# Performance work log

Measured on AMD Instinct MI355X. Metric: run time of the kernel, lower is better.

The kernel has to match this reference:

```python
import jax, jax.numpy as jnp
import numpy as np

B, T, DEMO = 64, 4096, 8
N_MOD, N_POS = 37, 10
D_IN = N_POS + 1 + N_MOD  # 48
PHI_W, LATENT = 128, 128
PSI_W, PSI_L = 128, 128
DOT, HEADS = 64, 4
RHO_W, OUT = 128, 1
MAX_TIME = 1000.0


def _dense_init(key, fan_in, fan_out):
    lim = float(np.sqrt(6.0 / fan_in))  # he_uniform-ish
    return jax.random.uniform(key, (fan_in, fan_out), jnp.float32, -lim, lim)


def setup_inputs() -> dict:
    key = jax.random.key(0)
    ks = jax.random.split(key, 32)
    inp = {}
    inp['demo'] = jax.random.normal(ks[0], (B, DEMO), jnp.float32)
    inp['times'] = jax.random.uniform(ks[1], (B, T, 1), jnp.float32, 0.0, 100.0)
    inp['values'] = jax.random.normal(ks[2], (B, T, 1), jnp.float32)
    inp['measurements'] = jax.random.randint(ks[3], (B, T), 0, N_MOD, jnp.int32)
    # all sequences full length -> N = B*(T+1) static
    inp['segment_ids'] = jnp.repeat(jnp.arange(B, dtype=jnp.int32), T + 1)
    inp['timescales'] = jnp.asarray(MAX_TIME ** np.linspace(0.0, 1.0, N_POS // 2), jnp.float32)
    inp['demo_W1'] = _dense_init(ks[4], DEMO, PHI_W); inp['demo_b1'] = jnp.zeros((PHI_W,), jnp.float32)
    inp['demo_W2'] = _dense_init(ks[5], PHI_W, D_IN); inp['demo_b2'] = jnp.zeros((D_IN,), jnp.float32)
    dims = [D_IN, PHI_W, PHI_W, PHI_W, LATENT]
    for i in range(4):
        inp['phi_W%d' % i] = _dense_init(ks[6 + i], dims[i], dims[i + 1])
        inp['phi_b%d' % i] = jnp.zeros((dims[i + 1],), jnp.float32)
    pdims = [D_IN, PSI_W, PSI_W, PSI_L]
    for i in range(3):
        inp['psi_W%d' % i] = _dense_init(ks[10 + i], pdims[i], pdims[i + 1])
        inp['psi_b%d' % i] = jnp.zeros((pdims[i + 1],), jnp.float32)
    inp['W_k'] = _dense_init(ks[13], PSI_L + D_IN, DOT * HEADS)
    # original inits W_q to zeros (degenerate uniform attention); small random keeps test non-trivial
    inp['W_q'] = jax.random.normal(ks[14], (HEADS, DOT), jnp.float32) * 0.05
    rdims = [LATENT * HEADS, RHO_W, RHO_W, RHO_W, OUT]
    for i in range(4):
        inp['rho_W%d' % i] = _dense_init(ks[15 + i], rdims[i], rdims[i + 1])
        inp['rho_b%d' % i] = jnp.zeros((rdims[i + 1],), jnp.float32)
    return inp


def _forward(demo, times, values, timescales,
             demo_W1, demo_b1, demo_W2, demo_b2,
             phi_W0, phi_b0, phi_W1, phi_b1, phi_W2, phi_b2, phi_W3, phi_b3,
             psi_W0, psi_b0, psi_W1, psi_b1, psi_W2, psi_b2,
             W_k, W_q,
             rho_W0, rho_b0, rho_W1, rho_b1, rho_W2, rho_b2, rho_W3, rho_b3,
             measurements, segment_ids):
    relu = jax.nn.relu
    nseg = demo.shape[0]
    # positional encoding: times [B,T,1] / timescales [5] -> sin|cos -> [B,T,10]
    scaled = times / timescales[None, None, :]
    tt = jnp.concatenate([jnp.sin(scaled), jnp.cos(scaled)], axis=-1)
    meas = jax.nn.one_hot(measurements, N_MOD, dtype=times.dtype)  # [B,T,37]
    combined = jnp.concatenate([tt, values, meas], axis=-1)        # [B,T,48]
    demo_enc = relu(demo @ demo_W1 + demo_b1) @ demo_W2 + demo_b2  # [B,48]
    x = jnp.concatenate([demo_enc[:, None, :], combined], axis=1)  # [B,T+1,48]
    collected = x.reshape(-1, x.shape[-1])                         # [N,48]
    # phi MLP -> encoded [N,LATENT]
    h = collected
    for W, b in ((phi_W0, phi_b0), (phi_W1, phi_b1), (phi_W2, phi_b2), (phi_W3, phi_b3)):
        h = relu(h @ W + b)
    encoded = h
    # psi MLP -> [N,PSI_L], then per-segment mean, scattered back
    p = collected
    for W, b in ((psi_W0, psi_b0), (psi_W1, psi_b1), (psi_W2, psi_b2)):
        p = relu(p @ W + b)
    seg_sum = jax.ops.segment_sum(p, segment_ids, num_segments=nseg)
    counts = jax.ops.segment_sum(jnp.ones((p.shape[0],), p.dtype), segment_ids, num_segments=nseg)
    agg = seg_sum / counts[:, None]
    comb2 = jnp.concatenate([collected, agg[segment_ids]], axis=-1)  # [N, 48+128]
    keys = (comb2 @ W_k).reshape(-1, HEADS, DOT)                     # [N,H,D]
    preattn = jnp.einsum('nhd,hd->nh', keys, W_q) / jnp.sqrt(jnp.float32(DOT))
    # segment softmax per head
    m = jax.ops.segment_max(preattn, segment_ids, num_segments=nseg)
    e = jnp.exp(preattn - m[segment_ids])
    s = jax.ops.segment_sum(e, segment_ids, num_segments=nseg)
    attn = e / s[segment_ids]                                        # [N,H]
    # head-major weighted concat: [N, H*LATENT]
    weighted = (attn[:, :, None] * encoded[:, None, :]).reshape(-1, HEADS * LATENT)
    agg_out = jax.ops.segment_sum(weighted, segment_ids, num_segments=nseg)  # [B,512]
    r = agg_out
    for W, b in ((rho_W0, rho_b0), (rho_W1, rho_b1), (rho_W2, rho_b2)):
        r = relu(r @ W + b)
    return jax.nn.sigmoid(r @ rho_W3 + rho_b3)  # [B,1]


def reference(demo, times, values, timescales,
              demo_W1, demo_b1, demo_W2, demo_b2,
              phi_W0, phi_b0, phi_W1, phi_b1, phi_W2, phi_b2, phi_W3, phi_b3,
              psi_W0, psi_b0, psi_W1, psi_b1, psi_W2, psi_b2,
              W_k, W_q,
              rho_W0, rho_b0, rho_W1, rho_b1, rho_W2, rho_b2, rho_W3, rho_b3,
              measurements, segment_ids):
    return _forward(demo, times, values, timescales,
                    demo_W1, demo_b1, demo_W2, demo_b2,
                    phi_W0, phi_b0, phi_W1, phi_b1, phi_W2, phi_b2, phi_W3, phi_b3,
                    psi_W0, psi_b0, psi_W1, psi_b1, psi_W2, psi_b2,
                    W_k, W_q,
                    rho_W0, rho_b0, rho_W1, rho_b1, rho_W2, rho_b2, rho_W3, rho_b3,
                    measurements, segment_ids)
```

## Files before the change

kernel.cpp:

```cpp
#include <hip/hip_runtime.h>
#include <hip/hip_bf16.h>
#include <math.h>


#define BSEG 64
#define TLEN 4096
#define NPART 9
#define PART_STRIDE 520

#define OFF_DEMO 0
#define OFF_WQ   3072
#define OFF_WT   3264
#define OFF_PARTIALS 31936

typedef __attribute__((ext_vector_type(8))) short short8;
typedef __attribute__((ext_vector_type(4))) float f32x4;

static __device__ __forceinline__ float bfbits2f(unsigned v) { return __uint_as_float(v << 16); }
static __device__ __forceinline__ unsigned short f2bf_rne(float x) {
  unsigned u = __float_as_uint(x);
  unsigned r = (u + 0x7FFFu + ((u >> 16) & 1u)) >> 16;
  return (unsigned short)r;
}
static __device__ __forceinline__ unsigned pk2(float a, float b) {
  float2 f2 = make_float2(a, b);
  __hip_bfloat162 h = __float22bfloat162_rn(f2);
  unsigned u;
  __builtin_memcpy(&u, &h, 4);
  return u;
}

__global__ __launch_bounds__(256) void k_prep(
    const float* __restrict__ demo, const float* __restrict__ dW1, const float* __restrict__ db1,
    const float* __restrict__ dW2, const float* __restrict__ db2,
    const float* __restrict__ Wk, const float* __restrict__ Wq,
    const float* __restrict__ W0, const float* __restrict__ W1,
    const float* __restrict__ W2, const float* __restrict__ W3,
    float* __restrict__ ws) {
  __shared__ float drow[8];
  __shared__ float hdrow[128];
  int bid = blockIdx.x, tid = threadIdx.x;
  if (bid < 224) {
    unsigned short* wt = (unsigned short*)(ws + OFF_WT);
    int i = bid * 256 + tid;
    float v;
    if (i < 8192) {
      int n = i >> 6, k = i & 63;
      v = (k < 48) ? W0[k * 128 + n] : 0.f;
    } else {
      int j = i - 8192;
      int l = j >> 14, r = j & 16383;
      int n = r >> 7, k = r & 127;
      const float* W = (l == 0) ? W1 : (l == 1) ? W2 : W3;
      v = W[k * 128 + n];
    }
    wt[i] = f2bf_rne(v);
    return;
  }
  if (bid == 224) {
    if (tid < 192) {
      int i = tid >> 2, h = tid & 3;
      float a = 0.f;
      for (int d = 0; d < 64; ++d) a = fmaf(Wk[i * 256 + h * 64 + d], Wq[h * 64 + d], a);
      ws[OFF_WQ + tid] = a * 0.125f;
    }
    return;
  }
  int r = bid - 225;
  if (tid < 8) drow[tid] = demo[r * 8 + tid];
  __syncthreads();
  if (tid < 128) {
    float a = db1[tid];
#pragma unroll
    for (int i = 0; i < 8; ++i) a = fmaf(drow[i], dW1[i * 128 + tid], a);
    hdrow[tid] = fmaxf(a, 0.f);
  }
  __syncthreads();
  if (tid < 48) {
    float a = db2[tid];
    for (int k = 0; k < 128; ++k) a = fmaf(hdrow[k], dW2[k * 48 + tid], a);
    ws[OFF_DEMO + r * 48 + tid] = a;
  }
}

static __device__ __forceinline__ void mfma_layer(
    const unsigned short* hin, unsigned short* hout,
    const short8 (&Bf)[2][4], const float (&bias)[2],
    int l16, int quad, int n0) {
#pragma unroll
  for (int mt = 0; mt < 4; ++mt) {
    short8 A[4];
#pragma unroll
    for (int s = 0; s < 4; ++s)
      A[s] = *(const short8*)(hin + (mt * 16 + l16) * 136 + s * 32 + quad * 8);
#pragma unroll
    for (int t = 0; t < 2; ++t) {
      f32x4 acc = {bias[t], bias[t], bias[t], bias[t]};
#pragma unroll
      for (int s = 0; s < 4; ++s)
        acc = __builtin_amdgcn_mfma_f32_16x16x32_bf16(A[s], Bf[t][s], acc, 0, 0, 0);
      int col = n0 + t * 16 + l16;
      int base = (mt * 16 + quad * 4) * 136 + col;
      unsigned u01 = pk2(fmaxf(acc[0], 0.f), fmaxf(acc[1], 0.f));
      unsigned u23 = pk2(fmaxf(acc[2], 0.f), fmaxf(acc[3], 0.f));
      hout[base]           = (unsigned short)u01;
      hout[base + 136]     = (unsigned short)(u01 >> 16);
      hout[base + 2 * 136] = (unsigned short)u23;
      hout[base + 3 * 136] = (unsigned short)(u23 >> 16);
    }
  }
}
static __device__ __forceinline__ void mfma_layer0(
    const unsigned short* cin, unsigned short* hout,
    const short8 (&B0)[2][2], const float (&bias0)[2],
    int l16, int quad, int n0) {
#pragma unroll
  for (int mt = 0; mt < 4; ++mt) {
    short8 A0[2];
#pragma unroll
    for (int s = 0; s < 2; ++s)
      A0[s] = *(const short8*)(cin + (mt * 16 + l16) * 72 + s * 32 + quad * 8);
#pragma unroll
    for (int t = 0; t < 2; ++t) {
      f32x4 acc = {bias0[t], bias0[t], bias0[t], bias0[t]};
      acc = __builtin_amdgcn_mfma_f32_16x16x32_bf16(A0[0], B0[t][0], acc, 0, 0, 0);
      acc = __builtin_amdgcn_mfma_f32_16x16x32_bf16(A0[1], B0[t][1], acc, 0, 0, 0);
      int col = n0 + t * 16 + l16;
      int base = (mt * 16 + quad * 4) * 136 + col;
      unsigned u01 = pk2(fmaxf(acc[0], 0.f), fmaxf(acc[1], 0.f));
      unsigned u23 = pk2(fmaxf(acc[2], 0.f), fmaxf(acc[3], 0.f));
      hout[base]           = (unsigned short)u01;
      hout[base + 136]     = (unsigned short)(u01 >> 16);
      hout[base + 2 * 136] = (unsigned short)u23;
      hout[base + 3 * 136] = (unsigned short)(u23 >> 16);
    }
  }
}

__global__ __launch_bounds__(256, 2) void k_main(
    const float* __restrict__ times, const float* __restrict__ values,
    const int* __restrict__ meas, const float* __restrict__ tsc,
    const float* __restrict__ ws,
    const float* __restrict__ b0g, const float* __restrict__ b1g,
    const float* __restrict__ b2g, const float* __restrict__ b3g,
    float* __restrict__ part) {
  __shared__ __align__(16) unsigned short hA[64 * 136];
  __shared__ __align__(16) unsigned short hB[64 * 136];
  __shared__ __align__(16) float elds[256];
  __shared__ float wql[192];
  int tid = threadIdx.x;
  const int lane = tid & 63, wv = tid >> 6, quad = lane >> 4, l16 = lane & 15;
  const int n0 = wv * 32;

  const unsigned short* wt = (const unsigned short*)(ws + OFF_WT);
  short8 B0[2][2], B1[2][4], B2[2][4], B3[2][4];
  float bias0[2], bias1[2], bias2[2], bias3[2];
#pragma unroll
  for (int t = 0; t < 2; ++t) {
    int n = n0 + t * 16 + l16;
    bias0[t] = b0g[n]; bias1[t] = b1g[n]; bias2[t] = b2g[n]; bias3[t] = b3g[n];
#pragma unroll
    for (int s = 0; s < 2; ++s)
      B0[t][s] = *(const short8*)(wt + n * 64 + s * 32 + quad * 8);
#pragma unroll
    for (int s = 0; s < 4; ++s) {
      B1[t][s] = *(const short8*)(wt + 8192  + n * 128 + s * 32 + quad * 8);
      B2[t][s] = *(const short8*)(wt + 24576 + n * 128 + s * 32 + quad * 8);
      B3[t][s] = *(const short8*)(wt + 40960 + n * 128 + s * 32 + quad * 8);
    }
  }
  if (tid < 192) wql[tid] = ws[OFF_WQ + tid];
  __syncthreads();

  if (blockIdx.x == 512) {
    {
      int r = tid >> 2, cs = tid & 3;
      unsigned short seg[16];
#pragma unroll
      for (int i = 0; i < 16; ++i) seg[i] = 0;
      if (cs < 3)
#pragma unroll
        for (int i = 0; i < 16; ++i) seg[i] = f2bf_rne(ws[OFF_DEMO + r * 48 + cs * 16 + i]);
      unsigned u[8];
#pragma unroll
      for (int i = 0; i < 8; ++i) u[i] = (unsigned)seg[2 * i] | ((unsigned)seg[2 * i + 1] << 16);
      uint4* dst = (uint4*)(hB + r * 72 + cs * 16);
      dst[0] = make_uint4(u[0], u[1], u[2], u[3]);
      dst[1] = make_uint4(u[4], u[5], u[6], u[7]);
    }
    {
      int r = tid >> 2, h = tid & 3;
      float a = 0.f;
      for (int i = 0; i < 48; ++i) a = fmaf(ws[OFF_DEMO + r * 48 + i], wql[i * 4 + h], a);
      elds[tid] = __expf(a);
    }
    __syncthreads();
    mfma_layer0(hB, hA, B0, bias0, l16, quad, n0); __syncthreads();
    mfma_layer(hA, hB, B1, bias1, l16, quad, n0); __syncthreads();
    mfma_layer(hB, hA, B2, bias2, l16, quad, n0); __syncthreads();
    mfma_layer(hA, hB, B3, bias3, l16, quad, n0); __syncthreads();
    {
      int r = tid >> 2, h = tid & 3;
      part[(r * NPART + 8) * PART_STRIDE + 4 + h] = elds[tid];
    }
    for (int i = tid; i < 64 * 512; i += 256) {
      int r = i >> 9, rem = i & 511;
      int h = rem >> 7, l = rem & 127;
      part[(r * NPART + 8) * PART_STRIDE + 8 + rem] =
          elds[r * 4 + h] * bfbits2f(hB[r * 136 + l]);
    }
    return;
  }

  int b = blockIdx.x >> 3, c = blockIdx.x & 7;
  int t0 = c << 9;
  float invts[5];
#pragma unroll
  for (int i = 0; i < 5; ++i) invts[i] = 1.f / tsc[i];

  float pacc[2][4] = {{0.f, 0.f, 0.f, 0.f}, {0.f, 0.f, 0.f, 0.f}};
  float sacc[4] = {0.f, 0.f, 0.f, 0.f};
  for (int tile = 0; tile < 8; ++tile) {
    int rb = tile << 6;
    {
      int r = tid >> 2, cs = tid & 3;
      int t = t0 + rb + r;
      int mm = meas[b * TLEN + t];
      unsigned short seg[16];
#pragma unroll
      for (int i = 0; i < 16; ++i) seg[i] = 0;
      if (cs == 0) {
        float tv = times[b * TLEN + t];
        float vvv = values[b * TLEN + t];
        float f[11];
#pragma unroll
        for (int i = 0; i < 5; ++i) {
          float s = tv * invts[i];
          f[i] = __sinf(s); f[5 + i] = __cosf(s);
          seg[i] = f2bf_rne(f[i]); seg[5 + i] = f2bf_rne(f[5 + i]);
        }
        f[10] = vvv;
        seg[10] = f2bf_rne(vvv);
#pragma unroll
        for (int h = 0; h < 4; ++h) {
          float a = wql[(11 + mm) * 4 + h];
#pragma unroll
          for (int i = 0; i < 11; ++i) a = fmaf(f[i], wql[i * 4 + h], a);
          elds[r * 4 + h] = __expf(a);
        }
      }
      int kk = 11 + mm;
      if ((kk >> 4) == cs) seg[kk & 15] = 0x3F80;
      unsigned u[8];
#pragma unroll
      for (int i = 0; i < 8; ++i) u[i] = (unsigned)seg[2 * i] | ((unsigned)seg[2 * i + 1] << 16);
      uint4* dst = (uint4*)(hB + r * 72 + cs * 16);
      dst[0] = make_uint4(u[0], u[1], u[2], u[3]);
      dst[1] = make_uint4(u[4], u[5], u[6], u[7]);
    }
    __syncthreads();
    mfma_layer0(hB, hA, B0, bias0, l16, quad, n0); __syncthreads();
    mfma_layer(hA, hB, B1, bias1, l16, quad, n0); __syncthreads();
    mfma_layer(hB, hA, B2, bias2, l16, quad, n0); __syncthreads();
#pragma unroll
    for (int mt = 0; mt < 4; ++mt) {
      short8 A[4];
#pragma unroll
      for (int s = 0; s < 4; ++s)
        A[s] = *(const short8*)(hA + (mt * 16 + l16) * 136 + s * 32 + quad * 8);
      f32x4 acc0 = {bias3[0], bias3[0], bias3[0], bias3[0]};
      f32x4 acc1 = {bias3[1], bias3[1], bias3[1], bias3[1]};
#pragma unroll
      for (int s = 0; s < 4; ++s) {
        acc0 = __builtin_amdgcn_mfma_f32_16x16x32_bf16(A[s], B3[0][s], acc0, 0, 0, 0);
        acc1 = __builtin_amdgcn_mfma_f32_16x16x32_bf16(A[s], B3[1][s], acc1, 0, 0, 0);
      }
#pragma unroll
      for (int j = 0; j < 4; ++j) {
        int lr = mt * 16 + quad * 4 + j;
        float4 e4 = *(const float4*)(elds + lr * 4);
        float v0 = fmaxf(acc0[j], 0.f), v1 = fmaxf(acc1[j], 0.f);
        pacc[0][0] = fmaf(v0, e4.x, pacc[0][0]);
        pacc[0][1] = fmaf(v0, e4.y, pacc[0][1]);
        pacc[0][2] = fmaf(v0, e4.z, pacc[0][2]);
        pacc[0][3] = fmaf(v0, e4.w, pacc[0][3]);
        pacc[1][0] = fmaf(v1, e4.x, pacc[1][0]);
        pacc[1][1] = fmaf(v1, e4.y, pacc[1][1]);
        pacc[1][2] = fmaf(v1, e4.z, pacc[1][2]);
        pacc[1][3] = fmaf(v1, e4.w, pacc[1][3]);
        sacc[0] += e4.x; sacc[1] += e4.y; sacc[2] += e4.z; sacc[3] += e4.w;
      }
    }
    __syncthreads();
  }
#pragma unroll
  for (int t = 0; t < 2; ++t)
#pragma unroll
    for (int h = 0; h < 4; ++h) {
      float v = pacc[t][h];
      v += __shfl_xor(v, 16, 64);
      v += __shfl_xor(v, 32, 64);
      pacc[t][h] = v;
    }
#pragma unroll
  for (int h = 0; h < 4; ++h) {
    float v = sacc[h];
    v += __shfl_xor(v, 16, 64);
    v += __shfl_xor(v, 32, 64);
    sacc[h] = v;
  }
  float* P = part + (b * NPART + c) * PART_STRIDE;
  if (tid < 4) P[4 + tid] = sacc[tid];
  if (quad == 0)
#pragma unroll
    for (int t = 0; t < 2; ++t)
#pragma unroll
      for (int h = 0; h < 4; ++h)
        P[8 + h * 128 + (n0 + t * 16 + l16)] = pacc[t][h];
}

__global__ __launch_bounds__(256) void k_combine(
    const float* __restrict__ part,
    const float* __restrict__ rW0, const float* __restrict__ rb0,
    const float* __restrict__ rW1, const float* __restrict__ rb1,
    const float* __restrict__ rW2, const float* __restrict__ rb2,
    const float* __restrict__ rW3, const float* __restrict__ rb3,
    float* __restrict__ out) {
  __shared__ float Ss[4], agg[512], r1[128], p0[256];
  int tid = threadIdx.x;
  int b = blockIdx.x;
  const float* P = part + b * NPART * PART_STRIDE;
  if (tid < 4) {
    float s = 0.f;
    for (int p = 0; p < NPART; ++p) s += P[p * PART_STRIDE + 4 + tid];
    Ss[tid] = s;
  }
  __syncthreads();
  for (int idx = tid; idx < 512; idx += 256) {
    int h = idx >> 7;
    float a = 0.f;
    for (int p = 0; p < NPART; ++p) a += P[p * PART_STRIDE + 8 + idx];
    agg[idx] = a / Ss[h];
  }
  __syncthreads();
  const int col = tid & 127, half = tid >> 7;
  {
    float a = 0.f;
    for (int k = half * 256; k < half * 256 + 256; ++k) a = fmaf(agg[k], rW0[k * 128 + col], a);
    p0[tid] = a;
  }
  __syncthreads();
  if (tid < 128) r1[tid] = fmaxf(rb0[tid] + p0[tid] + p0[128 + tid], 0.f);
  __syncthreads();
  {
    float a = 0.f;
    for (int k = half * 64; k < half * 64 + 64; ++k) a = fmaf(r1[k], rW1[k * 128 + col], a);
    p0[tid] = a;
  }
  __syncthreads();
  if (tid < 128) r1[tid] = fmaxf(rb1[tid] + p0[tid] + p0[128 + tid], 0.f);
  __syncthreads();
  {
    float a = 0.f;
    for (int k = half * 64; k < half * 64 + 64; ++k) a = fmaf(r1[k], rW2[k * 128 + col], a);
    p0[tid] = a;
  }
  __syncthreads();
  if (tid < 128) p0[tid] = fmaxf(rb2[tid] + p0[tid] + p0[128 + tid], 0.f) * rW3[tid];
  __syncthreads();
  if (tid < 64) {
    float v = p0[tid] + p0[tid + 64];
#pragma unroll
    for (int off = 32; off > 0; off >>= 1) v += __shfl_xor(v, off, 64);
    if (tid == 0) out[b] = 1.f / (1.f + __expf(-(rb3[0] + v)));
  }
}

extern "C" void kernel_launch(void* const* d_in, const int* in_sizes, int n_in,
                              void* d_out, int out_size, void* d_ws, size_t ws_size,
                              hipStream_t stream) {
  const float* demo   = (const float*)d_in[0];
  const float* times  = (const float*)d_in[1];
  const float* values = (const float*)d_in[2];
  const int*   meas   = (const int*)d_in[3];
  const float* tsc = (const float*)d_in[5];
  const float* dW1 = (const float*)d_in[6];
  const float* db1 = (const float*)d_in[7];
  const float* dW2 = (const float*)d_in[8];
  const float* db2 = (const float*)d_in[9];
  const float* pW0 = (const float*)d_in[10];
  const float* pb0 = (const float*)d_in[11];
  const float* pW1 = (const float*)d_in[12];
  const float* pb1 = (const float*)d_in[13];
  const float* pW2 = (const float*)d_in[14];
  const float* pb2 = (const float*)d_in[15];
  const float* pW3 = (const float*)d_in[16];
  const float* pb3 = (const float*)d_in[17];
  const float* Wk  = (const float*)d_in[24];
  const float* Wq  = (const float*)d_in[25];
  const float* rW0 = (const float*)d_in[26];
  const float* rb0 = (const float*)d_in[27];
  const float* rW1 = (const float*)d_in[28];
  const float* rb1 = (const float*)d_in[29];
  const float* rW2 = (const float*)d_in[30];
  const float* rb2 = (const float*)d_in[31];
  const float* rW3 = (const float*)d_in[32];
  const float* rb3 = (const float*)d_in[33];
  float* ws = (float*)d_ws;
  float* partials = ws + OFF_PARTIALS;

  k_prep<<<289, 256, 0, stream>>>(demo, dW1, db1, dW2, db2, Wk, Wq,
                                  pW0, pW1, pW2, pW3, ws);
  k_main<<<513, 256, 0, stream>>>(times, values, meas, tsc, ws,
                                  pb0, pb1, pb2, pb3, partials);
  k_combine<<<64, 256, 0, stream>>>(partials, rW0, rb0, rW1, rb1, rW2, rb2, rW3, rb3,
                                    (float*)d_out);
}
```

Before: 193.5 us.

## Precompute attention weights upfront and double-buffer layer-0 input tile construction

All 512 attention exponentials per block are computed in a prologue using all 256 threads, replacing the per-tile computation done by one thread in four. The per-block denominator sums are now reduced across the whole workgroup. The layer-0 input tile is double-buffered: the next tile is built while the current layer-0 MFMA runs, which also removes one barrier per tile. The cost is about 18 KB of extra LDS per block, which may lower occupancy below the two blocks per CU the launch bounds ask for, plus a prologue that reads the global inputs a second time.

```diff
diff --git a/kernel.cpp b/kernel.cpp
--- a/kernel.cpp
+++ b/kernel.cpp
@@ -146,8 +146,11 @@
     float* __restrict__ part) {
   __shared__ __align__(16) unsigned short hA[64 * 136];
   __shared__ __align__(16) unsigned short hB[64 * 136];
-  __shared__ __align__(16) float elds[256];
+  __shared__ __align__(16) unsigned short c0a[64 * 72];
+  __shared__ __align__(16) unsigned short c0b[64 * 72];
+  __shared__ __align__(16) float preb[512 * 4];
   __shared__ float wql[192];
+  __shared__ float mred[16];
   int tid = threadIdx.x;
   const int lane = tid & 63, wv = tid >> 6, quad = lane >> 4, l16 = lane & 15;
   const int n0 = wv * 32;
@@ -184,7 +187,7 @@
       unsigned u[8];
 #pragma unroll
       for (int i = 0; i < 8; ++i) u[i] = (unsigned)seg[2 * i] | ((unsigned)seg[2 * i + 1] << 16);
-      uint4* dst = (uint4*)(hB + r * 72 + cs * 16);
+      uint4* dst = (uint4*)(c0a + r * 72 + cs * 16);
       dst[0] = make_uint4(u[0], u[1], u[2], u[3]);
       dst[1] = make_uint4(u[4], u[5], u[6], u[7]);
     }
@@ -192,22 +195,22 @@
       int r = tid >> 2, h = tid & 3;
       float a = 0.f;
       for (int i = 0; i < 48; ++i) a = fmaf(ws[OFF_DEMO + r * 48 + i], wql[i * 4 + h], a);
-      elds[tid] = __expf(a);
+      preb[tid] = __expf(a);
     }
     __syncthreads();
-    mfma_layer0(hB, hA, B0, bias0, l16, quad, n0); __syncthreads();
+    mfma_layer0(c0a, hA, B0, bias0, l16, quad, n0); __syncthreads();
     mfma_layer(hA, hB, B1, bias1, l16, quad, n0); __syncthreads();
     mfma_layer(hB, hA, B2, bias2, l16, quad, n0); __syncthreads();
     mfma_layer(hA, hB, B3, bias3, l16, quad, n0); __syncthreads();
     {
       int r = tid >> 2, h = tid & 3;
-      part[(r * NPART + 8) * PART_STRIDE + 4 + h] = elds[tid];
+      part[(r * NPART + 8) * PART_STRIDE + 4 + h] = preb[tid];
     }
     for (int i = tid; i < 64 * 512; i += 256) {
       int r = i >> 9, rem = i & 511;
       int h = rem >> 7, l = rem & 127;
       part[(r * NPART + 8) * PART_STRIDE + 8 + rem] =
-          elds[r * 4 + h] * bfbits2f(hB[r * 136 + l]);
+          preb[r * 4 + h] * bfbits2f(hB[r * 136 + l]);
     }
     return;
   }
@@ -218,48 +221,67 @@
 #pragma unroll
   for (int i = 0; i < 5; ++i) invts[i] = 1.f / tsc[i];
 
+  float s4[4] = {0.f, 0.f, 0.f, 0.f};
+  for (int rr = 0; rr < 2; ++rr) {
+    int r = tid + rr * 256;
+    int t = t0 + r;
+    float tv = times[b * TLEN + t];
+    float vvv = values[b * TLEN + t];
+    int mm = meas[b * TLEN + t];
+    float f[11];
+#pragma unroll
+    for (int i = 0; i < 5; ++i) { float s = tv * invts[i]; f[i] = __sinf(s); f[5 + i] = __cosf(s); }
+    f[10] = vvv;
+#pragma unroll
+    for (int h = 0; h < 4; ++h) {
+      float a = wql[(11 + mm) * 4 + h];
+#pragma unroll
+      for (int i = 0; i < 11; ++i) a = fmaf(f[i], wql[i * 4 + h], a);
+      float e = __expf(a);
+      preb[r * 4 + h] = e;
+      s4[h] += e;
+    }
+  }
+
+#define BUILD_TILE(buf, rbase)                                                  \
+  do {                                                                          \
+    int r_ = tid >> 2, cs_ = tid & 3;                                           \
+    int t_ = t0 + (rbase) + r_;                                                 \
+    int mm_ = meas[b * TLEN + t_];                                              \
+    unsigned short seg_[16];                                                    \
+    _Pragma("unroll") for (int i_ = 0; i_ < 16; ++i_) seg_[i_] = 0;             \
+    if (cs_ == 0) {                                                             \
+      float tv_ = times[b * TLEN + t_];                                         \
+      float vv_ = values[b * TLEN + t_];                                        \
+      _Pragma("unroll") for (int i_ = 0; i_ < 5; ++i_) {                        \
+        float s_ = tv_ * invts[i_];                                             \
+        seg_[i_] = f2bf_rne(__sinf(s_)); seg_[5 + i_] = f2bf_rne(__cosf(s_));   \
+      }                                                                         \
+      seg_[10] = f2bf_rne(vv_);                                                 \
+    }                                                                           \
+    int kk_ = 11 + mm_;                                                         \
+    if ((kk_ >> 4) == cs_) seg_[kk_ & 15] = 0x3F80;                             \
+    unsigned u_[8];                                                             \
+    _Pragma("unroll") for (int i_ = 0; i_ < 8; ++i_)                            \
+      u_[i_] = (unsigned)seg_[2 * i_] | ((unsigned)seg_[2 * i_ + 1] << 16);     \
+    uint4* dst_ = (uint4*)((buf) + r_ * 72 + cs_ * 16);                         \
+    dst_[0] = make_uint4(u_[0], u_[1], u_[2], u_[3]);                           \
+    dst_[1] = make_uint4(u_[4], u_[5], u_[6], u_[7]);                           \
+  } while (0)
+
+  BUILD_TILE(c0a, 0);
+
   float pacc[2][4] = {{0.f, 0.f, 0.f, 0.f}, {0.f, 0.f, 0.f, 0.f}};
-  float sacc[4] = {0.f, 0.f, 0.f, 0.f};
   for (int tile = 0; tile < 8; ++tile) {
     int rb = tile << 6;
-    {
-      int r = tid >> 2, cs = tid & 3;
-      int t = t0 + rb + r;
-      int mm = meas[b * TLEN + t];
-      unsigned short seg[16];
-#pragma unroll
-      for (int i = 0; i < 16; ++i) seg[i] = 0;
-      if (cs == 0) {
-        float tv = times[b * TLEN + t];
-        float vvv = values[b * TLEN + t];
-        float f[11];
-#pragma unroll
-        for (int i = 0; i < 5; ++i) {
-          float s = tv * invts[i];
-          f[i] = __sinf(s); f[5 + i] = __cosf(s);
-          seg[i] = f2bf_rne(f[i]); seg[5 + i] = f2bf_rne(f[5 + i]);
-        }
-        f[10] = vvv;
-        seg[10] = f2bf_rne(vvv);
-#pragma unroll
-        for (int h = 0; h < 4; ++h) {
-          float a = wql[(11 + mm) * 4 + h];
-#pragma unroll
-          for (int i = 0; i < 11; ++i) a = fmaf(f[i], wql[i * 4 + h], a);
-          elds[r * 4 + h] = __expf(a);
-        }
-      }
-      int kk = 11 + mm;
-      if ((kk >> 4) == cs) seg[kk & 15] = 0x3F80;
-      unsigned u[8];
-#pragma unroll
-      for (int i = 0; i < 8; ++i) u[i] = (unsigned)seg[2 * i] | ((unsigned)seg[2 * i + 1] << 16);
-      uint4* dst = (uint4*)(hB + r * 72 + cs * 16);
-      dst[0] = make_uint4(u[0], u[1], u[2], u[3]);
-      dst[1] = make_uint4(u[4], u[5], u[6], u[7]);
-    }
     __syncthreads();
-    mfma_layer0(hB, hA, B0, bias0, l16, quad, n0); __syncthreads();
+    const unsigned short* cin = (tile & 1) ? c0b : c0a;
+    mfma_layer0(cin, hA, B0, bias0, l16, quad, n0);
+    if (tile < 7) {
+      unsigned short* nbuf = (tile & 1) ? c0a : c0b;
+      BUILD_TILE(nbuf, rb + 64);
+    }
+    __syncthreads();
     mfma_layer(hA, hB, B1, bias1, l16, quad, n0); __syncthreads();
     mfma_layer(hB, hA, B2, bias2, l16, quad, n0); __syncthreads();
 #pragma unroll
@@ -277,8 +299,8 @@
       }
 #pragma unroll
       for (int j = 0; j < 4; ++j) {
-        int lr = mt * 16 + quad * 4 + j;
-        float4 e4 = *(const float4*)(elds + lr * 4);
+        int row = rb + mt * 16 + quad * 4 + j;
+        float4 e4 = *(const float4*)(preb + row * 4);
         float v0 = fmaxf(acc0[j], 0.f), v1 = fmaxf(acc1[j], 0.f);
         pacc[0][0] = fmaf(v0, e4.x, pacc[0][0]);
         pacc[0][1] = fmaf(v0, e4.y, pacc[0][1]);
@@ -288,10 +310,8 @@
         pacc[1][1] = fmaf(v1, e4.y, pacc[1][1]);
         pacc[1][2] = fmaf(v1, e4.z, pacc[1][2]);
         pacc[1][3] = fmaf(v1, e4.w, pacc[1][3]);
-        sacc[0] += e4.x; sacc[1] += e4.y; sacc[2] += e4.z; sacc[3] += e4.w;
       }
     }
-    __syncthreads();
   }
 #pragma unroll
   for (int t = 0; t < 2; ++t)
@@ -303,14 +323,15 @@
       pacc[t][h] = v;
     }
 #pragma unroll
-  for (int h = 0; h < 4; ++h) {
-    float v = sacc[h];
-    v += __shfl_xor(v, 16, 64);
-    v += __shfl_xor(v, 32, 64);
-    sacc[h] = v;
-  }
+  for (int off = 32; off > 0; off >>= 1)
+#pragma unroll
+    for (int h = 0; h < 4; ++h) s4[h] += __shfl_xor(s4[h], off, 64);
+  if (lane == 0)
+#pragma unroll
+    for (int h = 0; h < 4; ++h) mred[wv * 4 + h] = s4[h];
+  __syncthreads();
   float* P = part + (b * NPART + c) * PART_STRIDE;
-  if (tid < 4) P[4 + tid] = sacc[tid];
+  if (tid < 4) P[4 + tid] = mred[tid] + mred[4 + tid] + mred[8 + tid] + mred[12 + tid];
   if (quad == 0)
 #pragma unroll
     for (int t = 0; t < 2; ++t)
```

Result: no change. 193.1 us (-0.2%).

## Transpose MFMA layers for vector LDS stores and precompute attention weights per chunk

Applied to the files above, without the earlier changes.

The hidden-layer MFMAs now swap operand roles (weights times activations), so each lane holds four consecutive neurons of one token. Each result is written back to LDS as a single 8-byte store instead of four scalar 16-bit stores, and biases are loaded as float4. The attention logits and their exponentials for all 512 rows of a chunk are computed once up front by all 256 threads, instead of by only a quarter of the threads inside each tile. The per-tile trailing barrier is removed and the exp sums are reduced by a wave shuffle plus a small LDS step. The cost is a larger LDS footprint (8 KB preb buffer), which may affect occupancy under the two-block launch bound.

```diff
diff --git a/kernel.cpp b/kernel.cpp
--- a/kernel.cpp
+++ b/kernel.cpp
@@ -83,56 +83,48 @@
   }
 }
 
-static __device__ __forceinline__ void mfma_layer(
+static __device__ __forceinline__ void mfma_layer_T(
     const unsigned short* hin, unsigned short* hout,
-    const short8 (&Bf)[2][4], const float (&bias)[2],
+    const short8 (&Wf)[2][4], const f32x4 (&bias4)[2],
     int l16, int quad, int n0) {
 #pragma unroll
   for (int mt = 0; mt < 4; ++mt) {
-    short8 A[4];
+    short8 Bv[4];
 #pragma unroll
     for (int s = 0; s < 4; ++s)
-      A[s] = *(const short8*)(hin + (mt * 16 + l16) * 136 + s * 32 + quad * 8);
+      Bv[s] = *(const short8*)(hin + (mt * 16 + l16) * 136 + s * 32 + quad * 8);
 #pragma unroll
     for (int t = 0; t < 2; ++t) {
-      f32x4 acc = {bias[t], bias[t], bias[t], bias[t]};
+      f32x4 acc = bias4[t];
 #pragma unroll
       for (int s = 0; s < 4; ++s)
-        acc = __builtin_amdgcn_mfma_f32_16x16x32_bf16(A[s], Bf[t][s], acc, 0, 0, 0);
-      int col = n0 + t * 16 + l16;
-      int base = (mt * 16 + quad * 4) * 136 + col;
+        acc = __builtin_amdgcn_mfma_f32_16x16x32_bf16(Wf[t][s], Bv[s], acc, 0, 0, 0);
       unsigned u01 = pk2(fmaxf(acc[0], 0.f), fmaxf(acc[1], 0.f));
       unsigned u23 = pk2(fmaxf(acc[2], 0.f), fmaxf(acc[3], 0.f));
-      hout[base]           = (unsigned short)u01;
-      hout[base + 136]     = (unsigned short)(u01 >> 16);
-      hout[base + 2 * 136] = (unsigned short)u23;
-      hout[base + 3 * 136] = (unsigned short)(u23 >> 16);
-    }
-  }
-}
-static __device__ __forceinline__ void mfma_layer0(
+      *(uint2*)(hout + (mt * 16 + l16) * 136 + n0 + t * 16 + quad * 4) =
+          make_uint2(u01, u23);
+    }
+  }
+}
+static __device__ __forceinline__ void mfma_layer0_T(
     const unsigned short* cin, unsigned short* hout,
-    const short8 (&B0)[2][2], const float (&bias0)[2],
+    const short8 (&Wf)[2][2], const f32x4 (&bias4)[2],
     int l16, int quad, int n0) {
 #pragma unroll
   for (int mt = 0; mt < 4; ++mt) {
-    short8 A0[2];
+    short8 Bv[2];
 #pragma unroll
     for (int s = 0; s < 2; ++s)
-      A0[s] = *(const short8*)(cin + (mt * 16 + l16) * 72 + s * 32 + quad * 8);
+      Bv[s] = *(const short8*)(cin + (mt * 16 + l16) * 72 + s * 32 + quad * 8);
 #pragma unroll
     for (int t = 0; t < 2; ++t) {
-      f32x4 acc = {bias0[t], bias0[t], bias0[t], bias0[t]};
-      acc = __builtin_amdgcn_mfma_f32_16x16x32_bf16(A0[0], B0[t][0], acc, 0, 0, 0);
-      acc = __builtin_amdgcn_mfma_f32_16x16x32_bf16(A0[1], B0[t][1], acc, 0, 0, 0);
-      int col = n0 + t * 16 + l16;
-      int base = (mt * 16 + quad * 4) * 136 + col;
+      f32x4 acc = bias4[t];
+      acc = __builtin_amdgcn_mfma_f32_16x16x32_bf16(Wf[t][0], Bv[0], acc, 0, 0, 0);
+      acc = __builtin_amdgcn_mfma_f32_16x16x32_bf16(Wf[t][1], Bv[1], acc, 0, 0, 0);
       unsigned u01 = pk2(fmaxf(acc[0], 0.f), fmaxf(acc[1], 0.f));
       unsigned u23 = pk2(fmaxf(acc[2], 0.f), fmaxf(acc[3], 0.f));
-      hout[base]           = (unsigned short)u01;
-      hout[base + 136]     = (unsigned short)(u01 >> 16);
-      hout[base + 2 * 136] = (unsigned short)u23;
-      hout[base + 3 * 136] = (unsigned short)(u23 >> 16);
+      *(uint2*)(hout + (mt * 16 + l16) * 136 + n0 + t * 16 + quad * 4) =
+          make_uint2(u01, u23);
     }
   }
 }
@@ -146,19 +138,25 @@
     float* __restrict__ part) {
   __shared__ __align__(16) unsigned short hA[64 * 136];
   __shared__ __align__(16) unsigned short hB[64 * 136];
-  __shared__ __align__(16) float elds[256];
+  __shared__ __align__(16) float preb[512 * 4];
   __shared__ float wql[192];
+  __shared__ float mred[16];
   int tid = threadIdx.x;
   const int lane = tid & 63, wv = tid >> 6, quad = lane >> 4, l16 = lane & 15;
   const int n0 = wv * 32;
 
   const unsigned short* wt = (const unsigned short*)(ws + OFF_WT);
   short8 B0[2][2], B1[2][4], B2[2][4], B3[2][4];
-  float bias0[2], bias1[2], bias2[2], bias3[2];
+  f32x4 bias0[2], bias1[2], bias2[2];
+  float bias3[2];
 #pragma unroll
   for (int t = 0; t < 2; ++t) {
     int n = n0 + t * 16 + l16;
-    bias0[t] = b0g[n]; bias1[t] = b1g[n]; bias2[t] = b2g[n]; bias3[t] = b3g[n];
+    int nq = n0 + t * 16 + quad * 4;
+    bias0[t] = *(const f32x4*)(b0g + nq);
+    bias1[t] = *(const f32x4*)(b1g + nq);
+    bias2[t] = *(const f32x4*)(b2g + nq);
+    bias3[t] = b3g[n];
 #pragma unroll
     for (int s = 0; s < 2; ++s)
       B0[t][s] = *(const short8*)(wt + n * 64 + s * 32 + quad * 8);
@@ -192,22 +190,25 @@
       int r = tid >> 2, h = tid & 3;
       float a = 0.f;
       for (int i = 0; i < 48; ++i) a = fmaf(ws[OFF_DEMO + r * 48 + i], wql[i * 4 + h], a);
-      elds[tid] = __expf(a);
-    }
+      preb[tid] = __expf(a);
+    }
+    f32x4 bias34[2];
+#pragma unroll
+    for (int t = 0; t < 2; ++t) bias34[t] = *(const f32x4*)(b3g + n0 + t * 16 + quad * 4);
     __syncthreads();
-    mfma_layer0(hB, hA, B0, bias0, l16, quad, n0); __syncthreads();
-    mfma_layer(hA, hB, B1, bias1, l16, quad, n0); __syncthreads();
-    mfma_layer(hB, hA, B2, bias2, l16, quad, n0); __syncthreads();
-    mfma_layer(hA, hB, B3, bias3, l16, quad, n0); __syncthreads();
+    mfma_layer0_T(hB, hA, B0, bias0, l16, quad, n0); __syncthreads();
+    mfma_layer_T(hA, hB, B1, bias1, l16, quad, n0); __syncthreads();
+    mfma_layer_T(hB, hA, B2, bias2, l16, quad, n0); __syncthreads();
+    mfma_layer_T(hA, hB, B3, bias34, l16, quad, n0); __syncthreads();
     {
       int r = tid >> 2, h = tid & 3;
-      part[(r * NPART + 8) * PART_STRIDE + 4 + h] = elds[tid];
+      part[(r * NPART + 8) * PART_STRIDE + 4 + h] = preb[tid];
     }
     for (int i = tid; i < 64 * 512; i += 256) {
       int r = i >> 9, rem = i & 511;
       int h = rem >> 7, l = rem & 127;
       part[(r * NPART + 8) * PART_STRIDE + 8 + rem] =
-          elds[r * 4 + h] * bfbits2f(hB[r * 136 + l]);
+          preb[r * 4 + h] * bfbits2f(hB[r * 136 + l]);
     }
     return;
   }
@@ -218,8 +219,29 @@
 #pragma unroll
   for (int i = 0; i < 5; ++i) invts[i] = 1.f / tsc[i];
 
+  float s4[4] = {0.f, 0.f, 0.f, 0.f};
+  for (int rr = 0; rr < 2; ++rr) {
+    int r = tid + rr * 256;
+    int t = t0 + r;
+    float tv = times[b * TLEN + t];
+    float vvv = values[b * TLEN + t];
+    int mm = meas[b * TLEN + t];
+    float f[11];
+#pragma unroll
+    for (int i = 0; i < 5; ++i) { float s = tv * invts[i]; f[i] = __sinf(s); f[5 + i] = __cosf(s); }
+    f[10] = vvv;
+#pragma unroll
+    for (int h = 0; h < 4; ++h) {
+      float a = wql[(11 + mm) * 4 + h];
+#pragma unroll
+      for (int i = 0; i < 11; ++i) a = fmaf(f[i], wql[i * 4 + h], a);
+      float e = __expf(a);
+      preb[r * 4 + h] = e;
+      s4[h] += e;
+    }
+  }
+
   float pacc[2][4] = {{0.f, 0.f, 0.f, 0.f}, {0.f, 0.f, 0.f, 0.f}};
-  float sacc[4] = {0.f, 0.f, 0.f, 0.f};
   for (int tile = 0; tile < 8; ++tile) {
     int rb = tile << 6;
     {
@@ -232,22 +254,13 @@
       if (cs == 0) {
         float tv = times[b * TLEN + t];
         float vvv = values[b * TLEN + t];
-        float f[11];
 #pragma unroll
         for (int i = 0; i < 5; ++i) {
           float s = tv * invts[i];
-          f[i] = __sinf(s); f[5 + i] = __cosf(s);
-          seg[i] = f2bf_rne(f[i]); seg[5 + i] = f2bf_rne(f[5 + i]);
+          seg[i] = f2bf_rne(__sinf(s));
+          seg[5 + i] = f2bf_rne(__cosf(s));
         }
-        f[10] = vvv;
         seg[10] = f2bf_rne(vvv);
-#pragma unroll
-        for (int h = 0; h < 4; ++h) {
-          float a = wql[(11 + mm) * 4 + h];
-#pragma unroll
-          for (int i = 0; i < 11; ++i) a = fmaf(f[i], wql[i * 4 + h], a);
-          elds[r * 4 + h] = __expf(a);
-        }
       }
       int kk = 11 + mm;
       if ((kk >> 4) == cs) seg[kk & 15] = 0x3F80;
@@ -259,9 +272,9 @@
       dst[1] = make_uint4(u[4], u[5], u[6], u[7]);
     }
     __syncthreads();
-    mfma_layer0(hB, hA, B0, bias0, l16, quad, n0); __syncthreads();
-    mfma_layer(hA, hB, B1, bias1, l16, quad, n0); __syncthreads();
-    mfma_layer(hB, hA, B2, bias2, l16, quad, n0); __syncthreads();
+    mfma_layer0_T(hB, hA, B0, bias0, l16, quad, n0); __syncthreads();
+    mfma_layer_T(hA, hB, B1, bias1, l16, quad, n0); __syncthreads();
+    mfma_layer_T(hB, hA, B2, bias2, l16, quad, n0); __syncthreads();
 #pragma unroll
     for (int mt = 0; mt < 4; ++mt) {
       short8 A[4];
@@ -277,8 +290,8 @@
       }
 #pragma unroll
       for (int j = 0; j < 4; ++j) {
-        int lr = mt * 16 + quad * 4 + j;
-        float4 e4 = *(const float4*)(elds + lr * 4);
+        int row = rb + mt * 16 + quad * 4 + j;
+        float4 e4 = *(const float4*)(preb + row * 4);
         float v0 = fmaxf(acc0[j], 0.f), v1 = fmaxf(acc1[j], 0.f);
         pacc[0][0] = fmaf(v0, e4.x, pacc[0][0]);
         pacc[0][1] = fmaf(v0, e4.y, pacc[0][1]);
@@ -288,10 +301,8 @@
         pacc[1][1] = fmaf(v1, e4.y, pacc[1][1]);
         pacc[1][2] = fmaf(v1, e4.z, pacc[1][2]);
         pacc[1][3] = fmaf(v1, e4.w, pacc[1][3]);
-        sacc[0] += e4.x; sacc[1] += e4.y; sacc[2] += e4.z; sacc[3] += e4.w;
       }
     }
-    __syncthreads();
   }
 #pragma unroll
   for (int t = 0; t < 2; ++t)
@@ -303,14 +314,15 @@
       pacc[t][h] = v;
     }
 #pragma unroll
-  for (int h = 0; h < 4; ++h) {
-    float v = sacc[h];
-    v += __shfl_xor(v, 16, 64);
-    v += __shfl_xor(v, 32, 64);
-    sacc[h] = v;
-  }
+  for (int off = 32; off > 0; off >>= 1)
+#pragma unroll
+    for (int h = 0; h < 4; ++h) s4[h] += __shfl_xor(s4[h], off, 64);
+  if (lane == 0)
+#pragma unroll
+    for (int h = 0; h < 4; ++h) mred[wv * 4 + h] = s4[h];
+  __syncthreads();
   float* P = part + (b * NPART + c) * PART_STRIDE;
-  if (tid < 4) P[4 + tid] = sacc[tid];
+  if (tid < 4) P[4 + tid] = mred[tid] + mred[4 + tid] + mred[8 + tid] + mred[12 + tid];
   if (quad == 0)
 #pragma unroll
     for (int t = 0; t < 2; ++t)
```

New measurement: 188.3 us. 1.03x faster.
